# Optimization experiments

Measured on AMD Instinct MI355X. Metric: run time of the kernel, lower is better.

## Reference

```python
import jax, jax.numpy as jnp
import numpy as np

B, N, K, C, D_IN, D_OUT = 64, 207, 32, 8, 64, 64


def setup_inputs() -> dict:
    key = jax.random.key(0)
    k1, k2, k3 = jax.random.split(key, 3)
    clustered_index_topk = jax.random.randint(k1, (B, N, K), 0, C)
    weightedDinput_topk = jax.random.normal(k2, (B, N, K, D_IN), dtype=jnp.float32)
    W = jax.random.normal(k3, (C, D_OUT, D_IN), dtype=jnp.float32) * 0.05
    return {"clustered_index_topk": clustered_index_topk,
            "weightedDinput_topk": weightedDinput_topk,
            "W": W}


def reference(clustered_index_topk, weightedDinput_topk, W):
    # one-hot over classes: [B, N, K, C]
    onehot = (clustered_index_topk[..., None] == jnp.arange(C)).astype(weightedDinput_topk.dtype)
    # per-class masked sum over top-k neighbors: [B, N, C, D_IN]
    sums = jnp.einsum('bnkc,bnkd->bncd', onehot, weightedDinput_topk)
    # per-class counts, clamped to >= 1 (matches torch.clamp(class_count, 1))
    counts = jnp.maximum(onehot.sum(axis=2), 1.0)  # [B, N, C]
    mean = sums / counts[..., None]
    # per-class Linear (weight [out, in], no bias) + Tanh -> [B, N, C, D_OUT]
    out = jnp.tanh(jnp.einsum('bncd,cod->bnco', mean, W))
    return out
```

## Files before the change

### kernel.cpp

```cpp
#include <hip/hip_runtime.h>
#include <cstddef>

#define BB 64
#define NN 207
#define KK 32
#define CC 8
#define DIN 64
#define DOUT 64
#define TILE 8
#define THREADS 128
#define NT ((NN + TILE - 1) / TILE)
#define MPAD 68

__device__ __forceinline__ float fast_tanh(float v) {
    float e = __expf(2.0f * v);
    return 1.0f - 2.0f * __builtin_amdgcn_rcpf(e + 1.0f);
}

__global__ __launch_bounds__(256) void transpose_W_kernel(
    const float* __restrict__ W, float* __restrict__ Wt)
{
    __shared__ float t[DIN * (DOUT + 1)];
    const int c   = blockIdx.x;
    const int tid = threadIdx.x;
    const float* __restrict__ Wc  = W  + (size_t)c * DOUT * DIN;
    float* __restrict__       Wtc = Wt + (size_t)c * DIN * DOUT;
    #pragma unroll
    for (int r = 0; r < 16; ++r) {
        const int i = r * 256 + tid;
        const int o = i >> 6, d = i & 63;
        t[d * (DOUT + 1) + o] = Wc[i];
    }
    __syncthreads();
    #pragma unroll
    for (int r = 0; r < 16; ++r) {
        const int i = r * 256 + tid;
        const int d = i >> 6, o = i & 63;
        Wtc[i] = t[d * (DOUT + 1) + o];
    }
}

__device__ __forceinline__ void pf8(float4 (&buf)[8],
                                    const float* __restrict__ xp, int g) {
    #pragma unroll
    for (int j = 0; j < 8; ++j)
        buf[j] = *(const float4*)(xp + (size_t)(g * 8 + j) * DIN);
}
__device__ __forceinline__ void cb8(float4 (&acc)[CC], const float4 (&buf)[8],
                                    const int* idx_row, int g) {
    #pragma unroll
    for (int j = 0; j < 8; ++j) {
        const int ca = idx_row[g * 8 + j];
        #pragma unroll
        for (int cc_ = 0; cc_ < CC; ++cc_) {
            const float mf = (ca == cc_) ? 1.0f : 0.0f;
            acc[cc_].x = fmaf(mf, buf[j].x, acc[cc_].x);
            acc[cc_].y = fmaf(mf, buf[j].y, acc[cc_].y);
            acc[cc_].z = fmaf(mf, buf[j].z, acc[cc_].z);
            acc[cc_].w = fmaf(mf, buf[j].w, acc[cc_].w);
        }
    }
}

__device__ __forceinline__ void wload(float4 (&w)[4],
                                      const float* __restrict__ Wtc, int dc) {
    #pragma unroll
    for (int j = 0; j < 4; ++j)
        w[j] = *(const float4*)(Wtc + (size_t)(dc * 4 + j) * DOUT);
}
__device__ __forceinline__ void wcompute(float4 (&acc2)[8], const float4 (&w)[4],
                                         const float* mean_base, int dc) {
    #pragma unroll
    for (int pp = 0; pp < 8; ++pp) {
        const float4 m = *(const float4*)(mean_base + (size_t)pp * CC * MPAD + dc * 4);
        acc2[pp].x = fmaf(m.x, w[0].x, acc2[pp].x);
        acc2[pp].y = fmaf(m.x, w[0].y, acc2[pp].y);
        acc2[pp].z = fmaf(m.x, w[0].z, acc2[pp].z);
        acc2[pp].w = fmaf(m.x, w[0].w, acc2[pp].w);
        acc2[pp].x = fmaf(m.y, w[1].x, acc2[pp].x);
        acc2[pp].y = fmaf(m.y, w[1].y, acc2[pp].y);
        acc2[pp].z = fmaf(m.y, w[1].z, acc2[pp].z);
        acc2[pp].w = fmaf(m.y, w[1].w, acc2[pp].w);
        acc2[pp].x = fmaf(m.z, w[2].x, acc2[pp].x);
        acc2[pp].y = fmaf(m.z, w[2].y, acc2[pp].y);
        acc2[pp].z = fmaf(m.z, w[2].z, acc2[pp].z);
        acc2[pp].w = fmaf(m.z, w[2].w, acc2[pp].w);
        acc2[pp].x = fmaf(m.w, w[3].x, acc2[pp].x);
        acc2[pp].y = fmaf(m.w, w[3].y, acc2[pp].y);
        acc2[pp].z = fmaf(m.w, w[3].z, acc2[pp].z);
        acc2[pp].w = fmaf(m.w, w[3].w, acc2[pp].w);
    }
}

template<bool USE_WT>
__global__ __launch_bounds__(THREADS, 4) void ordered_gcn_kernel(
    const int* __restrict__ idx,
    const float* __restrict__ x,
    const float* __restrict__ W,
    const float* __restrict__ Wt,
    float* __restrict__ out)
{
    __shared__ int   idx_s[TILE * KK];
    __shared__ float inv_s[TILE * CC];
    __shared__ float mean_s[TILE * CC * MPAD];

    const int tid = threadIdx.x;
    const int b  = blockIdx.y;
    const int n0 = blockIdx.x * TILE;

    #pragma unroll
    for (int r = 0; r < 2; ++r) {
        const int i = r * THREADS + tid;
        const int pq = i >> 5, k = i & 31;
        int n = n0 + pq; if (n > NN - 1) n = NN - 1;
        idx_s[i] = idx[((size_t)(b * NN + n)) * KK + k];
    }
    __syncthreads();

    if (tid < TILE * CC) {
        const int pp = tid >> 3, c = tid & 7;
        int cnt = 0;
        #pragma unroll
        for (int k = 0; k < KK; ++k) cnt += (idx_s[pp * KK + k] == c) ? 1 : 0;
        inv_s[tid] = 1.0f / (float)(cnt > 1 ? cnt : 1);
    }

    const int p  = tid >> 4;
    const int d4 = (tid & 15) * 4;
    {
        int n = n0 + p; if (n > NN - 1) n = NN - 1;
        const float* __restrict__ xp = x + ((size_t)(b * NN + n)) * KK * DIN + d4;
        const int* idx_row = &idx_s[p * KK];

        float4 acc[CC];
        #pragma unroll
        for (int c = 0; c < CC; ++c) acc[c] = make_float4(0.f, 0.f, 0.f, 0.f);

        float4 va[8], vb[8];
        pf8(va, xp, 0);
        pf8(vb, xp, 1);
        cb8(acc, va, idx_row, 0);
        pf8(va, xp, 2);
        cb8(acc, vb, idx_row, 1);
        pf8(vb, xp, 3);
        cb8(acc, va, idx_row, 2);
        cb8(acc, vb, idx_row, 3);

        __syncthreads();

        #pragma unroll
        for (int cc_ = 0; cc_ < CC; ++cc_) {
            const float s = inv_s[p * CC + cc_];
            float4 m;
            m.x = acc[cc_].x * s; m.y = acc[cc_].y * s;
            m.z = acc[cc_].z * s; m.w = acc[cc_].w * s;
            *(float4*)(&mean_s[(p * CC + cc_) * MPAD + d4]) = m;
        }
    }
    __syncthreads();

    {
        const int c  = (tid >> 4) & 7;
        const int o0 = (tid & 15) * 4;

        float4 acc2[8];
        #pragma unroll
        for (int pp = 0; pp < 8; ++pp) acc2[pp] = make_float4(0.f, 0.f, 0.f, 0.f);

        if (USE_WT) {
            const float* __restrict__ Wtc = Wt + (size_t)c * DIN * DOUT + o0;
            const float* mean_base = &mean_s[c * MPAD];

            float4 wa[4], wb[4];
            wload(wa, Wtc, 0);
            #pragma unroll 1
            for (int dc = 0; dc < 14; dc += 2) {
                wload(wb, Wtc, dc + 1);
                wcompute(acc2, wa, mean_base, dc);
                wload(wa, Wtc, dc + 2);
                wcompute(acc2, wb, mean_base, dc + 1);
            }
            wload(wb, Wtc, 15);
            wcompute(acc2, wa, mean_base, 14);
            wcompute(acc2, wb, mean_base, 15);
        } else {
            const float* __restrict__ Wc = W + (size_t)c * DOUT * DIN;
            #pragma unroll 1
            for (int dc = 0; dc < 16; ++dc) {
                float4 w[4];
                #pragma unroll
                for (int j = 0; j < 4; ++j)
                    w[j] = *(const float4*)(Wc + (size_t)(o0 + j) * DIN + dc * 4);
                #pragma unroll
                for (int pp = 0; pp < 8; ++pp) {
                    const float4 m = *(const float4*)(&mean_s[(pp * CC + c) * MPAD + dc * 4]);
                    float* a = (float*)&acc2[pp];
                    #pragma unroll
                    for (int j = 0; j < 4; ++j) {
                        a[j] = fmaf(m.x, w[j].x, a[j]);
                        a[j] = fmaf(m.y, w[j].y, a[j]);
                        a[j] = fmaf(m.z, w[j].z, a[j]);
                        a[j] = fmaf(m.w, w[j].w, a[j]);
                    }
                }
            }
        }

        #pragma unroll
        for (int pp = 0; pp < 8; ++pp) {
            const int nn = n0 + pp;
            if (nn < NN) {
                float4 r;
                r.x = fast_tanh(acc2[pp].x);
                r.y = fast_tanh(acc2[pp].y);
                r.z = fast_tanh(acc2[pp].z);
                r.w = fast_tanh(acc2[pp].w);
                *(float4*)(out + (((size_t)(b * NN + nn)) * CC + c) * DOUT + o0) = r;
            }
        }
    }
}

extern "C" void kernel_launch(void* const* d_in, const int* in_sizes, int n_in,
                              void* d_out, int out_size, void* d_ws, size_t ws_size,
                              hipStream_t stream) {
    const int*   idx = (const int*)d_in[0];
    const float* x   = (const float*)d_in[1];
    const float* W   = (const float*)d_in[2];
    float* out = (float*)d_out;
    float* Wt  = (float*)d_ws;
    dim3 grid(NT, BB);
    dim3 block(THREADS);
    const size_t wt_bytes = (size_t)CC * DIN * DOUT * sizeof(float);
    if (ws_size >= wt_bytes) {
        transpose_W_kernel<<<dim3(CC), dim3(256), 0, stream>>>(W, Wt);
        ordered_gcn_kernel<true><<<grid, block, 0, stream>>>(idx, x, W, Wt, out);
    } else {
        ordered_gcn_kernel<false><<<grid, block, 0, stream>>>(idx, x, W, Wt, out);
    }
}
```

Measured before the change: 190.7 us.

## Enlarge node tile to 32 with 256 threads and 16 nodes per thread in GEMM

```diff
diff --git a/kernel.cpp b/kernel.cpp
--- a/kernel.cpp
+++ b/kernel.cpp
@@ -7,8 +7,8 @@
 #define CC 8
 #define DIN 64
 #define DOUT 64
-#define TILE 8
-#define THREADS 128
+#define TILE 32
+#define THREADS 256
 #define NT ((NN + TILE - 1) / TILE)
 #define MPAD 68
 
@@ -68,10 +68,10 @@
     for (int j = 0; j < 4; ++j)
         w[j] = *(const float4*)(Wtc + (size_t)(dc * 4 + j) * DOUT);
 }
-__device__ __forceinline__ void wcompute(float4 (&acc2)[8], const float4 (&w)[4],
-                                         const float* mean_base, int dc) {
-    #pragma unroll
-    for (int pp = 0; pp < 8; ++pp) {
+__device__ __forceinline__ void wcompute16(float4 (&acc2)[16], const float4 (&w)[4],
+                                           const float* mean_base, int dc) {
+    #pragma unroll
+    for (int pp = 0; pp < 16; ++pp) {
         const float4 m = *(const float4*)(mean_base + (size_t)pp * CC * MPAD + dc * 4);
         acc2[pp].x = fmaf(m.x, w[0].x, acc2[pp].x);
         acc2[pp].y = fmaf(m.x, w[0].y, acc2[pp].y);
@@ -93,7 +93,7 @@
 }
 
 template<bool USE_WT>
-__global__ __launch_bounds__(THREADS, 4) void ordered_gcn_kernel(
+__global__ __launch_bounds__(THREADS, 2) void ordered_gcn_kernel(
     const int* __restrict__ idx,
     const float* __restrict__ x,
     const float* __restrict__ W,
@@ -109,7 +109,7 @@
     const int n0 = blockIdx.x * TILE;
 
     #pragma unroll
-    for (int r = 0; r < 2; ++r) {
+    for (int r = 0; r < 4; ++r) {
         const int i = r * THREADS + tid;
         const int pq = i >> 5, k = i & 31;
         int n = n0 + pq; if (n > NN - 1) n = NN - 1;
@@ -117,7 +117,7 @@
     }
     __syncthreads();
 
-    if (tid < TILE * CC) {
+    {
         const int pp = tid >> 3, c = tid & 7;
         int cnt = 0;
         #pragma unroll
@@ -128,61 +128,71 @@
     const int p  = tid >> 4;
     const int d4 = (tid & 15) * 4;
     {
-        int n = n0 + p; if (n > NN - 1) n = NN - 1;
-        const float* __restrict__ xp = x + ((size_t)(b * NN + n)) * KK * DIN + d4;
-        const int* idx_row = &idx_s[p * KK];
-
-        float4 acc[CC];
-        #pragma unroll
-        for (int c = 0; c < CC; ++c) acc[c] = make_float4(0.f, 0.f, 0.f, 0.f);
-
-        float4 va[8], vb[8];
-        pf8(va, xp, 0);
-        pf8(vb, xp, 1);
-        cb8(acc, va, idx_row, 0);
-        pf8(va, xp, 2);
-        cb8(acc, vb, idx_row, 1);
-        pf8(vb, xp, 3);
-        cb8(acc, va, idx_row, 2);
-        cb8(acc, vb, idx_row, 3);
+        int na = n0 + p;      if (na > NN - 1) na = NN - 1;
+        int nb = n0 + p + 16; if (nb > NN - 1) nb = NN - 1;
+        const float* __restrict__ xpa = x + ((size_t)(b * NN + na)) * KK * DIN + d4;
+        const float* __restrict__ xpb = x + ((size_t)(b * NN + nb)) * KK * DIN + d4;
+        const int* idx_row_a = &idx_s[p * KK];
+        const int* idx_row_b = &idx_s[(p + 16) * KK];
+
+        float4 acc0[CC], acc1[CC];
+        #pragma unroll
+        for (int c = 0; c < CC; ++c) {
+            acc0[c] = make_float4(0.f, 0.f, 0.f, 0.f);
+            acc1[c] = make_float4(0.f, 0.f, 0.f, 0.f);
+        }
+
+        #pragma unroll 1
+        for (int g = 0; g < 4; ++g) {
+            float4 va[8], vb[8];
+            pf8(va, xpa, g);
+            pf8(vb, xpb, g);
+            cb8(acc0, va, idx_row_a, g);
+            cb8(acc1, vb, idx_row_b, g);
+        }
 
         __syncthreads();
 
         #pragma unroll
         for (int cc_ = 0; cc_ < CC; ++cc_) {
-            const float s = inv_s[p * CC + cc_];
-            float4 m;
-            m.x = acc[cc_].x * s; m.y = acc[cc_].y * s;
-            m.z = acc[cc_].z * s; m.w = acc[cc_].w * s;
-            *(float4*)(&mean_s[(p * CC + cc_) * MPAD + d4]) = m;
+            const float s0 = inv_s[p * CC + cc_];
+            const float s1 = inv_s[(p + 16) * CC + cc_];
+            float4 m0, m1;
+            m0.x = acc0[cc_].x * s0; m0.y = acc0[cc_].y * s0;
+            m0.z = acc0[cc_].z * s0; m0.w = acc0[cc_].w * s0;
+            m1.x = acc1[cc_].x * s1; m1.y = acc1[cc_].y * s1;
+            m1.z = acc1[cc_].z * s1; m1.w = acc1[cc_].w * s1;
+            *(float4*)(&mean_s[(p * CC + cc_) * MPAD + d4]) = m0;
+            *(float4*)(&mean_s[((p + 16) * CC + cc_) * MPAD + d4]) = m1;
         }
     }
     __syncthreads();
 
     {
+        const int ph = tid >> 7;
         const int c  = (tid >> 4) & 7;
         const int o0 = (tid & 15) * 4;
 
-        float4 acc2[8];
-        #pragma unroll
-        for (int pp = 0; pp < 8; ++pp) acc2[pp] = make_float4(0.f, 0.f, 0.f, 0.f);
+        float4 acc2[16];
+        #pragma unroll
+        for (int pp = 0; pp < 16; ++pp) acc2[pp] = make_float4(0.f, 0.f, 0.f, 0.f);
 
         if (USE_WT) {
             const float* __restrict__ Wtc = Wt + (size_t)c * DIN * DOUT + o0;
-            const float* mean_base = &mean_s[c * MPAD];
+            const float* mean_base = &mean_s[(ph * 16 * CC + c) * MPAD];
 
             float4 wa[4], wb[4];
             wload(wa, Wtc, 0);
             #pragma unroll 1
             for (int dc = 0; dc < 14; dc += 2) {
                 wload(wb, Wtc, dc + 1);
-                wcompute(acc2, wa, mean_base, dc);
+                wcompute16(acc2, wa, mean_base, dc);
                 wload(wa, Wtc, dc + 2);
-                wcompute(acc2, wb, mean_base, dc + 1);
+                wcompute16(acc2, wb, mean_base, dc + 1);
             }
             wload(wb, Wtc, 15);
-            wcompute(acc2, wa, mean_base, 14);
-            wcompute(acc2, wb, mean_base, 15);
+            wcompute16(acc2, wa, mean_base, 14);
+            wcompute16(acc2, wb, mean_base, 15);
         } else {
             const float* __restrict__ Wc = W + (size_t)c * DOUT * DIN;
             #pragma unroll 1
@@ -192,8 +202,9 @@
                 for (int j = 0; j < 4; ++j)
                     w[j] = *(const float4*)(Wc + (size_t)(o0 + j) * DIN + dc * 4);
                 #pragma unroll
-                for (int pp = 0; pp < 8; ++pp) {
-                    const float4 m = *(const float4*)(&mean_s[(pp * CC + c) * MPAD + dc * 4]);
+                for (int pp = 0; pp < 16; ++pp) {
+                    const int pq = ph * 16 + pp;
+                    const float4 m = *(const float4*)(&mean_s[(pq * CC + c) * MPAD + dc * 4]);
                     float* a = (float*)&acc2[pp];
                     #pragma unroll
                     for (int j = 0; j < 4; ++j) {
@@ -207,8 +218,9 @@
         }
 
         #pragma unroll
-        for (int pp = 0; pp < 8; ++pp) {
-            const int nn = n0 + pp;
+        for (int pp = 0; pp < 16; ++pp) {
+            const int pq = ph * 16 + pp;
+            const int nn = n0 + pq;
             if (nn < NN) {
                 float4 r;
                 r.x = fast_tanh(acc2[pp].x);
```

New measurement: 186.7 us. -2.1%, faster.
